# Performance work log

Measured on AMD Instinct MI355X. Metric: run time of the kernel, lower is better.

Reference implementation:

```python
import jax, jax.numpy as jnp
import numpy as np

E, D, P, T = 65536, 256, 4, 9
N_TYPES, N_SRC = 14, 4
# base-type order: nmos, pmos, balun, resistor, capacitor, inductor, vsource, isource, port
N_PARAMS = np.array([2, 2, 1, 1, 1, 1, 3, 2, 4], dtype=np.int32)
_S = np.ones((T, P), dtype=np.float32)
_S[0, 1] = 1e-6   # nmos w
_S[1, 1] = 1e-6   # pmos w
_S[3, 0] = 1e3    # resistor r
_S[4, 0] = 1e-12  # capacitor c
_S[5, 0] = 1e-9   # inductor l
_S[7, 0] = 1e-3   # isource dc
_S[7, 1] = 1e-3   # isource mag
_S[8, 2] = 1e9    # port freq
SCALES = jnp.asarray(_S)


def setup_inputs() -> dict:
    key = jax.random.key(0)
    ks = jax.random.split(key, 12)
    base_ids = jax.random.randint(ks[0], (E,), 0, T)
    type_ids = jax.random.randint(ks[1], (E,), 0, N_TYPES)
    source_ids = jax.random.randint(ks[2], (E,), 0, N_SRC)
    # raw params at physically realistic magnitude (pre-division values ~ scale)
    params = jax.random.uniform(ks[3], (E, P), jnp.float32) * SCALES[base_ids]
    W1 = jax.random.normal(ks[4], (T, P, D), jnp.float32) * 0.1
    # zero weight rows beyond each expert's param arity (matches torch pad/truncate)
    arity_mask = (np.arange(P)[None, :] < N_PARAMS[:, None]).astype(np.float32)
    W1 = W1 * jnp.asarray(arity_mask)[:, :, None]
    b1 = jax.random.normal(ks[5], (T, D), jnp.float32) * 0.1
    W2 = jax.random.normal(ks[6], (T, D, D), jnp.float32) * 0.05
    b2 = jax.random.normal(ks[7], (T, D), jnp.float32) * 0.05
    Wf = jax.random.normal(ks[8], (3 * D, D), jnp.float32) * 0.05
    bf = jax.random.normal(ks[9], (D,), jnp.float32) * 0.05
    type_embed = jax.random.normal(ks[10], (N_TYPES, D), jnp.float32)
    source_embed = jax.random.normal(ks[11], (N_SRC, D), jnp.float32)
    return {"type_ids": type_ids, "source_ids": source_ids, "base_ids": base_ids,
            "params": params, "type_embed": type_embed, "source_embed": source_embed,
            "W1": W1, "b1": b1, "W2": W2, "b2": b2, "Wf": Wf, "bf": bf}


def reference(type_ids, source_ids, base_ids, params, type_embed, source_embed,
              W1, b1, W2, b2, Wf, bf):
    # per-edge scale division (SCALE_FACTORS)
    x = params / SCALES[base_ids]                       # [E, P]
    # expert layer 1: gather tiny [P,D] weights per edge
    h = jax.nn.relu(jnp.einsum('ep,epd->ed', x, W1[base_ids]) + b1[base_ids])  # [E, D]
    # expert layer 2: masked per-type GEMMs (T is small/fixed)
    pv = jnp.zeros_like(h)
    for t in range(T):
        pv = jnp.where((base_ids == t)[:, None], h @ W2[t] + b2[t], pv)
    concat = jnp.concatenate([type_embed[type_ids], source_embed[source_ids], pv], axis=-1)  # [E, 3D]
    return jax.nn.relu(concat @ Wf + bf)                # [E, D]
```

## Files before the change

### kernel.cpp

```cpp
#include <hip/hip_runtime.h>

#define E_N 65536
#define T_N 9

typedef __bf16 bf16x8 __attribute__((ext_vector_type(8)));
typedef float f32x4 __attribute__((ext_vector_type(4)));
typedef unsigned short ushort8 __attribute__((ext_vector_type(8)));
union U8 { ushort8 u; bf16x8 b; };
union BF2 { __bf16 h[2]; unsigned int u; };

#define OFF_CB   0
#define OFF_ABC  294912
#define OFF_D2   309248
#define OFF_CNT  311552
#define OFF_IDX  311712
#define WS_NEED_BYTES ((size_t)(311712 + 589824) * 4)

__device__ __constant__ float SCALES_C[9][4] = {
  {1.f,    1e-6f, 1.f,  1.f},
  {1.f,    1e-6f, 1.f,  1.f},
  {1.f,    1.f,   1.f,  1.f},
  {1e3f,   1.f,   1.f,  1.f},
  {1e-12f, 1.f,   1.f,  1.f},
  {1e-9f,  1.f,   1.f,  1.f},
  {1.f,    1.f,   1.f,  1.f},
  {1e-3f,  1e-3f, 1.f,  1.f},
  {1.f,    1.f,   1e9f, 1.f},
};

__device__ inline unsigned short f2bf(float f) {
  unsigned int u = __float_as_uint(f);
  unsigned int r = (u + 0x7FFFu + ((u >> 16) & 1u)) >> 16;
  return (unsigned short)r;
}

struct ScatSM { int sph[9][4]; int sbase[9]; };
struct EmbSM  { float partf[4 * 64 * 4]; };
struct CSM    { float w2s[8][256]; float partf[3 * 8 * 64 * 4]; };
union PrepSM  { ScatSM s; EmbSM e; CSM c; };

__global__ __launch_bounds__(256) void k_prep(
    const int* __restrict__ base_ids, const int* __restrict__ type_ids,
    const int* __restrict__ source_ids,
    const float* __restrict__ te, const float* __restrict__ se,
    const float* __restrict__ b2, const float* __restrict__ Wf,
    const float* __restrict__ bfv, const float* __restrict__ W2,
    int* __restrict__ cnt, int* __restrict__ idxArr,
    unsigned short* __restrict__ Cb,
    float* __restrict__ ABc, float* __restrict__ D2b) {
  __shared__ PrepSM sm;
  int b = blockIdx.x;
  int tid = threadIdx.x;
  int lane = tid & 63;
  int w = tid >> 6;

  if (b < 256) {
    int e = (b << 8) + tid;
    int bt = base_ids[e];
    int pk = e | (type_ids[e] << 16) | (source_ids[e] << 20);
    unsigned long long lanebit = 1ull << lane;

    #pragma unroll 1
    for (int t = 0; t < T_N; ++t) {
      unsigned long long m = __ballot(bt == t);
      if (lane == 0) sm.s.sph[t][w] = __popcll(m);
    }
    __syncthreads();
    if (tid < T_N) {
      int c0 = sm.s.sph[tid][0], c1 = sm.s.sph[tid][1];
      int c2 = sm.s.sph[tid][2], c3 = sm.s.sph[tid][3];
      int tot = c0 + c1 + c2 + c3;
      int base = (tot > 0) ? atomicAdd(&cnt[tid << 4], tot) : 0;
      sm.s.sbase[tid] = base;
      sm.s.sph[tid][0] = 0;
      sm.s.sph[tid][1] = c0;
      sm.s.sph[tid][2] = c0 + c1;
      sm.s.sph[tid][3] = c0 + c1 + c2;
    }
    __syncthreads();
    #pragma unroll 1
    for (int t = 0; t < T_N; ++t) {
      unsigned long long m = __ballot(bt == t);
      if (bt == t) {
        int pos = sm.s.sbase[t] + sm.s.sph[t][w] + __popcll(m & (lanebit - 1ull));
        idxArr[t * E_N + pos] = pk;
      }
    }
  } else if (b < 321) {
    int bb = b - 256;
    int dg = lane << 2;
    f32x4 acc0 = {0.f, 0.f, 0.f, 0.f}, acc1 = {0.f, 0.f, 0.f, 0.f};
    if (bb < 56) {
      int ty = bb >> 2, sr = bb & 3;
      const float* src = (w < 2) ? (te + ty * 256) : (se + sr * 256 - 256);
      int kbase = w << 7;
      #pragma unroll 8
      for (int k = kbase; k < kbase + 128; k += 2) {
        f32x4 wv0 = *(const f32x4*)&Wf[((k + 0) << 8) + dg];
        f32x4 wv1 = *(const f32x4*)&Wf[((k + 1) << 8) + dg];
        float e0 = src[k], e1 = src[k + 1];
        acc0.x = fmaf(e0, wv0.x, acc0.x); acc0.y = fmaf(e0, wv0.y, acc0.y);
        acc0.z = fmaf(e0, wv0.z, acc0.z); acc0.w = fmaf(e0, wv0.w, acc0.w);
        acc1.x = fmaf(e1, wv1.x, acc1.x); acc1.y = fmaf(e1, wv1.y, acc1.y);
        acc1.z = fmaf(e1, wv1.z, acc1.z); acc1.w = fmaf(e1, wv1.w, acc1.w);
      }
    } else {
      int t = bb - 56;
      const float* bp = b2 + t * 256;
      int kbase = w << 6;
      #pragma unroll 8
      for (int k = kbase; k < kbase + 64; k += 2) {
        f32x4 wv0 = *(const f32x4*)&Wf[((512 + k + 0) << 8) + dg];
        f32x4 wv1 = *(const f32x4*)&Wf[((512 + k + 1) << 8) + dg];
        float e0 = bp[k], e1 = bp[k + 1];
        acc0.x = fmaf(e0, wv0.x, acc0.x); acc0.y = fmaf(e0, wv0.y, acc0.y);
        acc0.z = fmaf(e0, wv0.z, acc0.z); acc0.w = fmaf(e0, wv0.w, acc0.w);
        acc1.x = fmaf(e1, wv1.x, acc1.x); acc1.y = fmaf(e1, wv1.y, acc1.y);
        acc1.z = fmaf(e1, wv1.z, acc1.z); acc1.w = fmaf(e1, wv1.w, acc1.w);
      }
    }
    acc0 += acc1;
    *(f32x4*)&sm.e.partf[((w << 6) + lane) << 2] = acc0;
    __syncthreads();
    if (w == 0) {
      acc0 += *(const f32x4*)&sm.e.partf[((1 << 6) + lane) << 2];
      acc0 += *(const f32x4*)&sm.e.partf[((2 << 6) + lane) << 2];
      acc0 += *(const f32x4*)&sm.e.partf[((3 << 6) + lane) << 2];
      if (bb < 56) {
        *(f32x4*)&ABc[(bb << 8) + dg] = acc0;
      } else {
        f32x4 bv = *(const f32x4*)&bfv[dg];
        *(f32x4*)&D2b[((bb - 56) << 8) + dg] = acc0 + bv;
      }
    }
  } else {
    int ci = b - 321;
    int t = ci >> 5;
    int j0 = (ci & 31) << 3;
    for (int i = tid; i < 2048; i += 256)
      sm.c.w2s[i >> 8][i & 255] =
          W2[(size_t)t * 65536 + (size_t)(j0 + (i >> 8)) * 256 + (i & 255)];
    __syncthreads();

    int dg = lane << 2;
    int kbase = w << 6;
    f32x4 acc[8];
    #pragma unroll
    for (int j = 0; j < 8; ++j) acc[j] = (f32x4){0.f, 0.f, 0.f, 0.f};
    #pragma unroll 2
    for (int k0 = 0; k0 < 64; k0 += 4) {
      f32x4 a[8];
      #pragma unroll
      for (int j = 0; j < 8; ++j) a[j] = *(const f32x4*)&sm.c.w2s[j][kbase + k0];
      #pragma unroll
      for (int kk = 0; kk < 4; ++kk) {
        f32x4 wv = *(const f32x4*)&Wf[((512 + kbase + k0 + kk) << 8) + dg];
        #pragma unroll
        for (int j = 0; j < 8; ++j) {
          float aj = a[j][kk];
          acc[j].x = fmaf(aj, wv.x, acc[j].x);
          acc[j].y = fmaf(aj, wv.y, acc[j].y);
          acc[j].z = fmaf(aj, wv.z, acc[j].z);
          acc[j].w = fmaf(aj, wv.w, acc[j].w);
        }
      }
    }
    if (w > 0) {
      #pragma unroll
      for (int j = 0; j < 8; ++j)
        *(f32x4*)&sm.c.partf[(((((w - 1) << 3) + j) << 6) + lane) << 2] = acc[j];
    }
    __syncthreads();
    if (w == 0) {
      #pragma unroll
      for (int p = 0; p < 3; ++p)
        #pragma unroll
        for (int j = 0; j < 8; ++j)
          acc[j] += *(const f32x4*)&sm.c.partf[((((p << 3) + j) << 6) + lane) << 2];
      unsigned short* CbT = Cb + (size_t)t * 65536;
      #pragma unroll
      for (int di = 0; di < 4; ++di) {
        ushort8 o;
        #pragma unroll
        for (int j = 0; j < 8; ++j) o[j] = f2bf(acc[j][di]);
        *(ushort8*)(CbT + ((size_t)((j0 >> 3) << 8) + dg + di) * 8) = o;
      }
    }
  }
}

__global__ __launch_bounds__(256, 4) void edge_gemm(
    const int* __restrict__ cnt, const int* __restrict__ idxArr,
    const float* __restrict__ params,
    const float* __restrict__ W1, const float* __restrict__ b1,
    const unsigned short* __restrict__ Cb, const float* __restrict__ ABc,
    const float* __restrict__ D2b, float* __restrict__ out) {
  int b = blockIdx.x;
  int t = -1, m0 = 0, n = 0;
  {
    int acc = 0;
    #pragma unroll
    for (int tt = 0; tt < T_N; ++tt) {
      int c = cnt[tt << 4];
      int nb = (c + 63) >> 6;
      if (t < 0 && b < acc + nb) { t = tt; m0 = (b - acc) << 6; n = c; }
      acc += nb;
    }
  }
  if (t < 0) return;

  __shared__ unsigned short hb[64 * 256];
  __shared__ int eidx[64];
  __shared__ float4 xs[64];

  int tid = threadIdx.x;
  int lane = tid & 63;
  int w = tid >> 6;
  int l15 = lane & 15;
  int l4 = lane >> 4;

  const unsigned short* CbT = Cb + (size_t)t * 65536;

  bf16x8 bcur[4];
  #pragma unroll
  for (int nn = 0; nn < 4; ++nn) {
    U8 u;
    u.u = *(const ushort8*)(CbT + (size_t)((l4 << 8) + (w << 6) + (nn << 4) + l15) * 8);
    bcur[nn] = u.b;
  }

  if (tid < 64) {
    int m = m0 + tid;
    int mc = (m < n) ? m : (n - 1);
    int pk = idxArr[(size_t)t * E_N + mc];
    eidx[tid] = pk;
    int e = pk & 0xFFFF;
    float4 pr = *(const float4*)(params + (size_t)e * 4);
    float4 x;
    x.x = pr.x / SCALES_C[t][0];
    x.y = pr.y / SCALES_C[t][1];
    x.z = pr.z / SCALES_C[t][2];
    x.w = pr.w / SCALES_C[t][3];
    xs[tid] = x;
  }
  __syncthreads();

  {
    int dp = tid & 127, mh = tid >> 7;
    int d0 = dp << 1;
    const float* W1t = W1 + t * 1024;
    float2 wq0 = *(const float2*)&W1t[d0];
    float2 wq1 = *(const float2*)&W1t[256 + d0];
    float2 wq2 = *(const float2*)&W1t[512 + d0];
    float2 wq3 = *(const float2*)&W1t[768 + d0];
    float2 bq  = *(const float2*)&b1[t * 256 + d0];
    int mb = mh << 5;
    #pragma unroll 4
    for (int i = 0; i < 32; ++i) {
      int m = mb + i;
      float4 x = xs[m];
      float h0 = fmaf(x.x, wq0.x, fmaf(x.y, wq1.x, fmaf(x.z, wq2.x, fmaf(x.w, wq3.x, bq.x))));
      float h1 = fmaf(x.x, wq0.y, fmaf(x.y, wq1.y, fmaf(x.z, wq2.y, fmaf(x.w, wq3.y, bq.y))));
      BF2 pk2;
      pk2.h[0] = (__bf16)fmaxf(h0, 0.f);
      pk2.h[1] = (__bf16)fmaxf(h1, 0.f);
      int off = (m << 9) + ((d0 << 1) ^ ((m & 7) << 4));
      *(unsigned int*)((char*)hb + off) = pk2.u;
    }
  }
  __syncthreads();

  f32x4 acc[4][4];
  #pragma unroll
  for (int i = 0; i < 4; ++i)
    #pragma unroll
    for (int j = 0; j < 4; ++j) acc[i][j] = (f32x4){0.f, 0.f, 0.f, 0.f};

  #pragma unroll 1
  for (int s = 0; s < 8; ++s) {
    bf16x8 bnext[4];
    int sn = (s + 1) & 7;
    #pragma unroll
    for (int nn = 0; nn < 4; ++nn) {
      int koct = (sn << 2) + l4;
      U8 u;
      u.u = *(const ushort8*)(CbT + (size_t)((koct << 8) + (w << 6) + (nn << 4) + l15) * 8);
      bnext[nn] = u.b;
    }
    #pragma unroll
    for (int mt = 0; mt < 4; ++mt) {
      int row = (mt << 4) + l15;
      int byte = (row << 9) + ((((s << 6) + (l4 << 4))) ^ ((row & 7) << 4));
      U8 a;
      a.u = *(const ushort8*)((const char*)hb + byte);
      #pragma unroll
      for (int nn = 0; nn < 4; ++nn)
        acc[mt][nn] = __builtin_amdgcn_mfma_f32_16x16x32_bf16(a.b, bcur[nn], acc[mt][nn], 0, 0, 0);
    }
    #pragma unroll
    for (int nn = 0; nn < 4; ++nn) bcur[nn] = bnext[nn];
  }

  float* fb = (float*)hb;
  const float* d2p = D2b + (t << 8);
  #pragma unroll
  for (int p = 0; p < 2; ++p) {
    __syncthreads();
    #pragma unroll
    for (int mh = 0; mh < 2; ++mh) {
      int mt = (p << 1) + mh;
      int lrb = (mh << 4) + (l4 << 2);
      #pragma unroll
      for (int nn = 0; nn < 4; ++nn) {
        int col = (w << 6) + (nn << 4) + l15;
        #pragma unroll
        for (int r = 0; r < 4; ++r) {
          int lr = lrb + r;
          fb[lr * 256 + (col ^ ((lr & 7) << 2))] = acc[mt][nn][r];
        }
      }
    }
    __syncthreads();
    int lr = tid >> 3;
    int c8 = tid & 7;
    int row_g = (p << 5) + lr;
    if (m0 + row_g < n) {
      int pk = eidx[row_g];
      int e = pk & 0xFFFF;
      int ty = (pk >> 16) & 15;
      int sr = (pk >> 20) & 3;
      const float* abp = ABc + (size_t)(((ty << 2) + sr) << 8);
      float* op = out + (size_t)e * 256;
      int sw = (lr & 7) << 2;
      #pragma unroll
      for (int v = 0; v < 8; ++v) {
        int col = (c8 << 2) + (v << 5);
        f32x4 vv = *(const f32x4*)&fb[lr * 256 + (col ^ sw)];
        f32x4 ab = *(const f32x4*)&abp[col];
        f32x4 d2 = *(const f32x4*)&d2p[col];
        f32x4 rr;
        rr.x = fmaxf(vv.x + ab.x + d2.x, 0.f);
        rr.y = fmaxf(vv.y + ab.y + d2.y, 0.f);
        rr.z = fmaxf(vv.z + ab.z + d2.z, 0.f);
        rr.w = fmaxf(vv.w + ab.w + d2.w, 0.f);
        *(f32x4*)&op[col] = rr;
      }
    }
  }
}

extern "C" void kernel_launch(void* const* d_in, const int* in_sizes, int n_in,
                              void* d_out, int out_size, void* d_ws, size_t ws_size,
                              hipStream_t stream) {
  const int*   type_ids   = (const int*)  d_in[0];
  const int*   source_ids = (const int*)  d_in[1];
  const int*   base_ids   = (const int*)  d_in[2];
  const float* params     = (const float*)d_in[3];
  const float* te         = (const float*)d_in[4];
  const float* se         = (const float*)d_in[5];
  const float* W1         = (const float*)d_in[6];
  const float* b1         = (const float*)d_in[7];
  const float* W2         = (const float*)d_in[8];
  const float* b2         = (const float*)d_in[9];
  const float* Wf         = (const float*)d_in[10];
  const float* bfv        = (const float*)d_in[11];
  float* out = (float*)d_out;

  if (ws_size < WS_NEED_BYTES) return;

  float* wsf = (float*)d_ws;
  unsigned short* Cb = (unsigned short*)(wsf + OFF_CB);
  float* ABc = wsf + OFF_ABC;
  float* D2b = wsf + OFF_D2;
  int*   cnt = (int*)(wsf + OFF_CNT);
  int*   idx = (int*)(wsf + OFF_IDX);

  hipMemsetAsync(cnt, 0, 160 * sizeof(int), stream);
  k_prep<<<609, 256, 0, stream>>>(base_ids, type_ids, source_ids, te, se, b2,
                                  Wf, bfv, W2, cnt, idx, Cb, ABc, D2b);
  edge_gemm<<<1033, 256, 0, stream>>>(cnt, idx, params, W1, b1, Cb, ABc, D2b, out);
}
```

Before: 61.78 us.

## Double edge-GEMM tile to 128 rows with 8 waves; read W2 directly in prep

```diff
diff --git a/kernel.cpp b/kernel.cpp
--- a/kernel.cpp
+++ b/kernel.cpp
@@ -36,7 +36,7 @@
 
 struct ScatSM { int sph[9][4]; int sbase[9]; };
 struct EmbSM  { float partf[4 * 64 * 4]; };
-struct CSM    { float w2s[8][256]; float partf[3 * 8 * 64 * 4]; };
+struct CSM    { float partf[3 * 8 * 64 * 4]; };
 union PrepSM  { ScatSM s; EmbSM e; CSM c; };
 
 __global__ __launch_bounds__(256) void k_prep(
@@ -137,10 +137,7 @@
     int ci = b - 321;
     int t = ci >> 5;
     int j0 = (ci & 31) << 3;
-    for (int i = tid; i < 2048; i += 256)
-      sm.c.w2s[i >> 8][i & 255] =
-          W2[(size_t)t * 65536 + (size_t)(j0 + (i >> 8)) * 256 + (i & 255)];
-    __syncthreads();
+    const float* W2t = W2 + (size_t)t * 65536 + (size_t)j0 * 256;
 
     int dg = lane << 2;
     int kbase = w << 6;
@@ -151,7 +148,10 @@
     for (int k0 = 0; k0 < 64; k0 += 4) {
       f32x4 a[8];
       #pragma unroll
-      for (int j = 0; j < 8; ++j) a[j] = *(const f32x4*)&sm.c.w2s[j][kbase + k0];
+      for (int j = 0; j < 8; ++j) {
+        int off = __builtin_amdgcn_readfirstlane((j << 8) + kbase + k0);
+        a[j] = *(const f32x4*)(W2t + off);
+      }
       #pragma unroll
       for (int kk = 0; kk < 4; ++kk) {
         f32x4 wv = *(const f32x4*)&Wf[((512 + kbase + k0 + kk) << 8) + dg];
@@ -189,7 +189,7 @@
   }
 }
 
-__global__ __launch_bounds__(256, 4) void edge_gemm(
+__global__ __launch_bounds__(512, 4) void edge_gemm(
     const int* __restrict__ cnt, const int* __restrict__ idxArr,
     const float* __restrict__ params,
     const float* __restrict__ W1, const float* __restrict__ b1,
@@ -202,34 +202,26 @@
     #pragma unroll
     for (int tt = 0; tt < T_N; ++tt) {
       int c = cnt[tt << 4];
-      int nb = (c + 63) >> 6;
-      if (t < 0 && b < acc + nb) { t = tt; m0 = (b - acc) << 6; n = c; }
+      int nb = (c + 127) >> 7;
+      if (t < 0 && b < acc + nb) { t = tt; m0 = (b - acc) << 7; n = c; }
       acc += nb;
     }
   }
   if (t < 0) return;
 
-  __shared__ unsigned short hb[64 * 256];
-  __shared__ int eidx[64];
-  __shared__ float4 xs[64];
+  __shared__ unsigned short hb[128 * 256];
+  __shared__ int eidx[128];
+  __shared__ float4 xs[128];
 
   int tid = threadIdx.x;
   int lane = tid & 63;
   int w = tid >> 6;
   int l15 = lane & 15;
   int l4 = lane >> 4;
-
-  const unsigned short* CbT = Cb + (size_t)t * 65536;
-
-  bf16x8 bcur[4];
-  #pragma unroll
-  for (int nn = 0; nn < 4; ++nn) {
-    U8 u;
-    u.u = *(const ushort8*)(CbT + (size_t)((l4 << 8) + (w << 6) + (nn << 4) + l15) * 8);
-    bcur[nn] = u.b;
-  }
-
-  if (tid < 64) {
+  int wm = w >> 2;
+  int wn = w & 3;
+
+  if (tid < 128) {
     int m = m0 + tid;
     int mc = (m < n) ? m : (n - 1);
     int pk = idxArr[(size_t)t * E_N + mc];
@@ -276,29 +268,31 @@
     #pragma unroll
     for (int j = 0; j < 4; ++j) acc[i][j] = (f32x4){0.f, 0.f, 0.f, 0.f};
 
+  const unsigned short* CbT = Cb + (size_t)t * 65536;
+
   #pragma unroll 1
   for (int s = 0; s < 8; ++s) {
-    bf16x8 bnext[4];
-    int sn = (s + 1) & 7;
+    bf16x8 bfr[4];
     #pragma unroll
     for (int nn = 0; nn < 4; ++nn) {
-      int koct = (sn << 2) + l4;
+      int koct = (s << 2) + l4;
+      int d = (wn << 6) + (nn << 4) + l15;
       U8 u;
-      u.u = *(const ushort8*)(CbT + (size_t)((koct << 8) + (w << 6) + (nn << 4) + l15) * 8);
-      bnext[nn] = u.b;
-    }
+      u.u = *(const ushort8*)(CbT + (size_t)((koct << 8) + d) * 8);
+      bfr[nn] = u.b;
+    }
+    __builtin_amdgcn_s_setprio(1);
     #pragma unroll
     for (int mt = 0; mt < 4; ++mt) {
-      int row = (mt << 4) + l15;
+      int row = (wm << 6) + (mt << 4) + l15;
       int byte = (row << 9) + ((((s << 6) + (l4 << 4))) ^ ((row & 7) << 4));
       U8 a;
       a.u = *(const ushort8*)((const char*)hb + byte);
       #pragma unroll
       for (int nn = 0; nn < 4; ++nn)
-        acc[mt][nn] = __builtin_amdgcn_mfma_f32_16x16x32_bf16(a.b, bcur[nn], acc[mt][nn], 0, 0, 0);
-    }
-    #pragma unroll
-    for (int nn = 0; nn < 4; ++nn) bcur[nn] = bnext[nn];
+        acc[mt][nn] = __builtin_amdgcn_mfma_f32_16x16x32_bf16(a.b, bfr[nn], acc[mt][nn], 0, 0, 0);
+    }
+    __builtin_amdgcn_s_setprio(0);
   }
 
   float* fb = (float*)hb;
@@ -306,24 +300,24 @@
   #pragma unroll
   for (int p = 0; p < 2; ++p) {
     __syncthreads();
-    #pragma unroll
-    for (int mh = 0; mh < 2; ++mh) {
-      int mt = (p << 1) + mh;
-      int lrb = (mh << 4) + (l4 << 2);
-      #pragma unroll
-      for (int nn = 0; nn < 4; ++nn) {
-        int col = (w << 6) + (nn << 4) + l15;
+    if (wm == p) {
+      #pragma unroll
+      for (int mt = 0; mt < 4; ++mt) {
         #pragma unroll
-        for (int r = 0; r < 4; ++r) {
-          int lr = lrb + r;
-          fb[lr * 256 + (col ^ ((lr & 7) << 2))] = acc[mt][nn][r];
+        for (int nn = 0; nn < 4; ++nn) {
+          int col = (wn << 6) + (nn << 4) + l15;
+          #pragma unroll
+          for (int r = 0; r < 4; ++r) {
+            int lr = (mt << 4) + (l4 << 2) + r;
+            fb[lr * 256 + (col ^ ((lr & 7) << 2))] = acc[mt][nn][r];
+          }
         }
       }
     }
     __syncthreads();
     int lr = tid >> 3;
     int c8 = tid & 7;
-    int row_g = (p << 5) + lr;
+    int row_g = (p << 6) + lr;
     if (m0 + row_g < n) {
       int pk = eidx[row_g];
       int e = pk & 0xFFFF;
@@ -378,5 +372,5 @@
   hipMemsetAsync(cnt, 0, 160 * sizeof(int), stream);
   k_prep<<<609, 256, 0, stream>>>(base_ids, type_ids, source_ids, te, se, b2,
                                   Wf, bfv, W2, cnt, idx, Cb, ABc, D2b);
-  edge_gemm<<<1033, 256, 0, stream>>>(cnt, idx, params, W1, b1, Cb, ABc, D2b, out);
+  edge_gemm<<<521, 512, 0, stream>>>(cnt, idx, params, W1, b1, Cb, ABc, D2b, out);
 }
```

After: 57.45 us. 7.0% less time.
